# Kernel optimization log

Measured on AMD Instinct MI355X. Metric: run time of the kernel, lower is better.

The kernel has to match this reference:

```python
import jax, jax.numpy as jnp
import numpy as np

B, H, W = 2, 240, 320
C_ENC, C_SEG = 64, 21
TRUNC = 3
REP = 2 * TRUNC + 1
DMIN, DMAX = 0.4, 6.0
VOXEL = 0.03
FDIMS = 256.0
FX = FY = 300.0


def _point_sample(feat, grid):
    # feat: [C, Hf, Wf]; grid: [N, 2] = (x, y) in [0, 1].
    # Matches F.grid_sample(feat, 2*grid-1, bilinear, zeros, align_corners=False).
    Cc, Hf, Wf = feat.shape
    ix = grid[:, 0] * Wf - 0.5
    iy = grid[:, 1] * Hf - 0.5
    x0 = jnp.floor(ix)
    y0 = jnp.floor(iy)
    wx = ix - x0
    wy = iy - y0

    def gather(xi, yi):
        valid = (xi >= 0) & (xi < Wf) & (yi >= 0) & (yi < Hf)
        xc = jnp.clip(xi, 0, Wf - 1).astype(jnp.int32)
        yc = jnp.clip(yi, 0, Hf - 1).astype(jnp.int32)
        return feat[:, yc, xc] * valid.astype(feat.dtype)

    return (gather(x0, y0) * ((1 - wx) * (1 - wy))
            + gather(x0 + 1, y0) * (wx * (1 - wy))
            + gather(x0, y0 + 1) * ((1 - wx) * wy)
            + gather(x0 + 1, y0 + 1) * (wx * wy))  # [C, N]


def _single(depth, enc, seg, intr):
    f32 = depth.dtype
    K_inv = jnp.linalg.inv(intr)

    # generate_frustum: image corners unprojected at depth_min / depth_max.
    cpx = jnp.array([[0., 0.], [W, 0.], [0., H], [W, H]], f32)

    def unproj(z):
        p = jnp.concatenate([cpx * z, jnp.full((4, 1), z, f32), jnp.ones((4, 1), f32)], -1)
        return (K_inv @ p.T).T[:, :3]

    corners = jnp.concatenate([unproj(DMIN), unproj(DMAX)], 0)  # [8, 3]
    fmin = corners.min(0)
    fmax = corners.max(0)
    # compute_camera2frustum_transform: scale to voxels, shift frustum min to origin.
    c2f = (jnp.eye(4, dtype=f32)
           .at[jnp.arange(3), jnp.arange(3)].set(1.0 / VOXEL)
           .at[:3, 3].set(-fmin / VOXEL))
    pad_off = (FDIMS - (fmax - fmin) / VOXEL) * 0.5  # [3]

    # depth clipping (dense mask instead of nonzero; invalid rows zeroed at end)
    valid = (depth >= DMIN) & (depth <= DMAX)
    z = jnp.where(valid, depth, 0.0).reshape(-1)  # [N]
    yy, xx = jnp.meshgrid(jnp.arange(H, dtype=f32), jnp.arange(W, dtype=f32), indexing='ij')
    xy = jnp.stack([xx.reshape(-1), yy.reshape(-1)], -1)  # [N, 2] (x, y)
    norm_xy = xy / jnp.array([W, H], f32)
    xv_yv = norm_xy * jnp.array([W, H], f32) * z[:, None]  # image_size = (W, H)
    feat_grid = xy / jnp.array([W, H], f32)  # feat_size covers full image

    pix = jnp.concatenate([xv_yv, z[:, None], jnp.ones_like(z)[:, None]], -1).T  # [4, N]
    gc = (c2f @ (K_inv @ pix)).T[:, :3]  # [N, 3] frustum-grid coords
    cz = gc[:, 2]
    offs = jnp.arange(-TRUNC, TRUNC + 1, dtype=f32)  # [REP]
    coords = gc[:, None, :] + offs[None, :, None] * jnp.array([0., 0., 1.], f32)
    flat_coords = coords.reshape(-1, 3) + pad_off  # [N*REP, 3]

    # truncated df values: frac(z) + offset, then sign/abs channels
    df = (cz - jnp.trunc(cz))[:, None] + offs[None, :]  # [N, REP]
    df = jnp.stack([jnp.sign(df), jnp.abs(df)], -1)  # [N, REP, 2]

    seg_f = _point_sample(seg, norm_xy).T   # [N, C_SEG]
    enc_f = _point_sample(enc, feat_grid).T  # [N, C_ENC]
    samp = jnp.concatenate([enc_f, seg_f], -1)  # [N, C_ENC+C_SEG]
    samp = jnp.broadcast_to(samp[:, None, :], (H * W, REP, C_ENC + C_SEG))
    feats = jnp.concatenate([df, samp], -1).reshape(-1, 2 + C_ENC + C_SEG)  # [N*REP, D]

    m = jnp.broadcast_to(valid.reshape(-1)[:, None], (H * W, REP)).reshape(-1, 1).astype(f32)
    return jnp.concatenate([feats * m, flat_coords * m], -1)  # [N*REP, D+3]


def setup_inputs() -> dict:
    key = jax.random.key(0)
    k1, k2, k3 = jax.random.split(key, 3)
    depth = jax.random.uniform(k1, (B, H, W), minval=0.2, maxval=6.2)
    enc = jax.random.normal(k2, (B, C_ENC, H // 2, W // 2), dtype=jnp.float32)
    seg = jax.random.normal(k3, (B, C_SEG, H, W), dtype=jnp.float32)
    K = np.eye(4, dtype=np.float32)
    K[0, 0] = FX; K[1, 1] = FY; K[0, 2] = W / 2.0; K[1, 2] = H / 2.0
    intrinsic = jnp.asarray(np.broadcast_to(K, (B, 4, 4)).copy())
    return {"depth": depth, "encoder_features": enc, "sem_seg": seg, "intrinsic": intrinsic}


def reference(depth, encoder_features, sem_seg, intrinsic):
    # [B, H*W*REP, 2 + C_ENC + C_SEG + 3] = sparse features ++ frustum coordinates
    return jax.vmap(_single)(depth, encoder_features, sem_seg, intrinsic)
```

## Files before the change

### kernel.cpp

```cpp
#include <hip/hip_runtime.h>
#include <math.h>

#define BPIX 64
#define HW   76800
#define W_   320
#define H_   240
#define ENC_W 160
#define ENC_H 120
#define CENC 64
#define CSEG 21
#define NCH  85
#define ROW  90
#define PIXF 630
#define TPLS 94
#define NF4  10080

typedef float f4v __attribute__((ext_vector_type(4)));

__global__ void setup_consts_kernel(const float* __restrict__ intr,
                                    float* __restrict__ C) {
  int b = threadIdx.x;
  if (b >= 2) return;
  float A[4][4], inv[4][4];
  for (int r = 0; r < 4; ++r)
    for (int c = 0; c < 4; ++c) {
      A[r][c] = intr[b * 16 + r * 4 + c];
      inv[r][c] = (r == c) ? 1.f : 0.f;
    }
  for (int k = 0; k < 4; ++k) {
    int piv = k; float best = fabsf(A[k][k]);
    for (int r = k + 1; r < 4; ++r) {
      float v = fabsf(A[r][k]);
      if (v > best) { best = v; piv = r; }
    }
    if (piv != k) {
      for (int c = 0; c < 4; ++c) {
        float t = A[k][c]; A[k][c] = A[piv][c]; A[piv][c] = t;
        t = inv[k][c]; inv[k][c] = inv[piv][c]; inv[piv][c] = t;
      }
    }
    float ip = 1.f / A[k][k];
    for (int c = 0; c < 4; ++c) { A[k][c] *= ip; inv[k][c] *= ip; }
    for (int r = 0; r < 4; ++r) if (r != k) {
      float f = A[r][k];
      for (int c = 0; c < 4; ++c) { A[r][c] -= f * A[k][c]; inv[r][c] -= f * inv[k][c]; }
    }
  }
  const float cpx[4][2] = {{0.f, 0.f}, {320.f, 0.f}, {0.f, 240.f}, {320.f, 240.f}};
  float fmn[3] = {1e30f, 1e30f, 1e30f}, fmx[3] = {-1e30f, -1e30f, -1e30f};
  for (int zi = 0; zi < 2; ++zi) {
    float z = zi ? 6.0f : 0.4f;
    for (int i = 0; i < 4; ++i) {
      float px = cpx[i][0] * z, py = cpx[i][1] * z;
      for (int ax = 0; ax < 3; ++ax) {
        float v = inv[ax][0] * px + inv[ax][1] * py + inv[ax][2] * z + inv[ax][3];
        fmn[ax] = fminf(fmn[ax], v);
        fmx[ax] = fmaxf(fmx[ax], v);
      }
    }
  }
  float* Cb = C + b * 32;
  for (int r = 0; r < 4; ++r)
    for (int c = 0; c < 4; ++c) Cb[r * 4 + c] = inv[r][c];
  for (int ax = 0; ax < 3; ++ax) {
    Cb[16 + ax] = -fmn[ax] / 0.03f;
    Cb[19 + ax] = (256.0f - (fmx[ax] - fmn[ax]) / 0.03f) * 0.5f;
  }
}

__global__ __launch_bounds__(256) void sparse_proj_kernel(
    const float* __restrict__ depth, const float* __restrict__ enc,
    const float* __restrict__ seg, const float* __restrict__ C,
    float* __restrict__ out) {
  __shared__ float  tpl[BPIX * TPLS];
  __shared__ float2 sd[BPIX * 7];
  __shared__ float  fcz[BPIX * 7];
  __shared__ float  mArr[BPIX];
  __shared__ int    eo0[BPIX], eo1[BPIX], eo2[BPIX], eo3[BPIX];
  __shared__ float  ew0[BPIX], ew1[BPIX], ew2[BPIX], ew3[BPIX];
  __shared__ int    so0[BPIX], so1[BPIX], so2[BPIX], so3[BPIX];
  __shared__ float  sw0[BPIX], sw1[BPIX], sw2[BPIX], sw3[BPIX];

  const int tid = threadIdx.x;
  const int bx  = blockIdx.x;
  const int b   = blockIdx.y;
  const float* Cb = C + b * 32;
  const int x0 = (bx % 5) * 64;
  const int yrow = bx / 5;

  const int grp = tid >> 6;
  const int p   = tid & 63;

  if (grp == 0) {
    const float d = depth[(size_t)b * HW + bx * BPIX + p];
    const bool val = (d >= 0.4f) && (d <= 6.0f);
    const float m = val ? 1.f : 0.f;
    const float z = val ? d : 0.f;
    const float nx = (float)(x0 + p) / 320.f;
    const float ny = (float)yrow / 240.f;
    const float xv = nx * 320.f * z;
    const float yv = ny * 240.f * z;
    const float q0 = Cb[0] * xv + Cb[1] * yv + Cb[2] * z + Cb[3];
    const float q1 = Cb[4] * xv + Cb[5] * yv + Cb[6] * z + Cb[7];
    const float q2 = Cb[8] * xv + Cb[9] * yv + Cb[10] * z + Cb[11];
    const float q3 = Cb[12] * xv + Cb[13] * yv + Cb[14] * z + Cb[15];
    const float INV_V = (float)(1.0 / 0.03);
    const float gcx = q0 * INV_V + Cb[16] * q3;
    const float gcy = q1 * INV_V + Cb[17] * q3;
    const float gcz = q2 * INV_V + Cb[18] * q3;
    mArr[p] = m;
    tpl[p * TPLS + 87] = (gcx + Cb[19]) * m;
    tpl[p * TPLS + 88] = (gcy + Cb[20]) * m;
    const float fr = gcz - truncf(gcz);
    const float fz = (gcz + Cb[21]) * m;
#pragma unroll
    for (int r = 0; r < 7; ++r) {
      const float df = fr + (float)(r - 3);
      const float s = (df > 0.f) ? 1.f : ((df < 0.f) ? -1.f : 0.f);
      sd[p * 7 + r] = make_float2(s * m, fabsf(df) * m);
      fcz[p * 7 + r] = fz + (float)(r - 3) * m;
    }
  } else if (grp == 1) {
    const float nx = (float)(x0 + p) / 320.f;
    const float ny = (float)yrow / 240.f;
    const float ix = nx * 160.f - 0.5f;
    const float iy = ny * 120.f - 0.5f;
    const float x0f = floorf(ix), y0f = floorf(iy);
    const float wx = ix - x0f, wy = iy - y0f;
    const int xi0 = (int)x0f, yi0 = (int)y0f;
    const int xi1 = xi0 + 1, yi1 = yi0 + 1;
    const float vx0 = (xi0 >= 0 && xi0 < ENC_W) ? 1.f : 0.f;
    const float vx1 = (xi1 >= 0 && xi1 < ENC_W) ? 1.f : 0.f;
    const float vy0 = (yi0 >= 0 && yi0 < ENC_H) ? 1.f : 0.f;
    const float vy1 = (yi1 >= 0 && yi1 < ENC_H) ? 1.f : 0.f;
    const int xc0 = min(max(xi0, 0), ENC_W - 1), xc1 = min(max(xi1, 0), ENC_W - 1);
    const int yc0 = min(max(yi0, 0), ENC_H - 1), yc1 = min(max(yi1, 0), ENC_H - 1);
    eo0[p] = yc0 * ENC_W + xc0; ew0[p] = (1.f - wx) * (1.f - wy) * vx0 * vy0;
    eo1[p] = yc0 * ENC_W + xc1; ew1[p] = wx * (1.f - wy) * vx1 * vy0;
    eo2[p] = yc1 * ENC_W + xc0; ew2[p] = (1.f - wx) * wy * vx0 * vy1;
    eo3[p] = yc1 * ENC_W + xc1; ew3[p] = wx * wy * vx1 * vy1;
  } else if (grp == 2) {
    const float nx = (float)(x0 + p) / 320.f;
    const float ny = (float)yrow / 240.f;
    const float ix = nx * 320.f - 0.5f;
    const float iy = ny * 240.f - 0.5f;
    const float x0f = floorf(ix), y0f = floorf(iy);
    const float wx = ix - x0f, wy = iy - y0f;
    const int xi0 = (int)x0f, yi0 = (int)y0f;
    const int xi1 = xi0 + 1, yi1 = yi0 + 1;
    const float vx0 = (xi0 >= 0 && xi0 < W_) ? 1.f : 0.f;
    const float vx1 = (xi1 >= 0 && xi1 < W_) ? 1.f : 0.f;
    const float vy0 = (yi0 >= 0 && yi0 < H_) ? 1.f : 0.f;
    const float vy1 = (yi1 >= 0 && yi1 < H_) ? 1.f : 0.f;
    const int xc0 = min(max(xi0, 0), W_ - 1), xc1 = min(max(xi1, 0), W_ - 1);
    const int yc0 = min(max(yi0, 0), H_ - 1), yc1 = min(max(yi1, 0), H_ - 1);
    so0[p] = yc0 * W_ + xc0; sw0[p] = (1.f - wx) * (1.f - wy) * vx0 * vy0;
    so1[p] = yc0 * W_ + xc1; sw1[p] = wx * (1.f - wy) * vx1 * vy0;
    so2[p] = yc1 * W_ + xc0; sw2[p] = (1.f - wx) * wy * vx0 * vy1;
    so3[p] = yc1 * W_ + xc1; sw3[p] = wx * wy * vx1 * vy1;
  }
  __syncthreads();

  for (int idx = tid; idx < BPIX * NCH; idx += 256) {
    const int pp = idx & (BPIX - 1);
    const int ch = idx >> 6;
    float v;
    if (ch < CENC) {
      const float* fb = enc + ((size_t)b * CENC + ch) * (ENC_H * ENC_W);
      v = ew0[pp] * fb[eo0[pp]] + ew1[pp] * fb[eo1[pp]] +
          ew2[pp] * fb[eo2[pp]] + ew3[pp] * fb[eo3[pp]];
    } else {
      const float* fb = seg + ((size_t)b * CSEG + (ch - CENC)) * (size_t)HW;
      v = sw0[pp] * fb[so0[pp]] + sw1[pp] * fb[so1[pp]] +
          sw2[pp] * fb[so2[pp]] + sw3[pp] * fb[so3[pp]];
    }
    tpl[pp * TPLS + 2 + ch] = v * mArr[pp];
  }
  __syncthreads();

  f4v* out4 = reinterpret_cast<f4v*>(out + (size_t)(b * HW + bx * BPIX) * PIXF);
  for (int j = tid; j < NF4; j += 256) {
    const unsigned e0 = (unsigned)j << 2;
    const int pq = (int)((e0 * 53262u) >> 25);
    const int w  = (int)e0 - pq * 630;
    const int r  = (int)(((unsigned)w * 729u) >> 16);
    const int c  = w - r * 90;
    f4v v;
    if ((unsigned)(c - 2) <= 83u) {
      const float2* t = reinterpret_cast<const float2*>(&tpl[pq * TPLS + c]);
      const float2 a = t[0];
      const float2 bq = t[1];
      v.x = a.x; v.y = a.y; v.z = bq.x; v.w = bq.y;
    } else {
#pragma unroll
      for (int k = 0; k < 4; ++k) {
        const unsigned e = e0 + (unsigned)k;
        const int pk = (int)((e * 53262u) >> 25);
        const int wk = (int)e - pk * 630;
        const int rk = (int)(((unsigned)wk * 729u) >> 16);
        const int ck = wk - rk * 90;
        float val;
        if (ck == 0)       val = sd[pk * 7 + rk].x;
        else if (ck == 1)  val = sd[pk * 7 + rk].y;
        else if (ck == 89) val = fcz[pk * 7 + rk];
        else               val = tpl[pk * TPLS + ck];
        v[k] = val;
      }
    }
    __builtin_nontemporal_store(v, &out4[j]);
  }
}

extern "C" void kernel_launch(void* const* d_in, const int* in_sizes, int n_in,
                              void* d_out, int out_size, void* d_ws, size_t ws_size,
                              hipStream_t stream) {
  const float* depth = (const float*)d_in[0];
  const float* enc   = (const float*)d_in[1];
  const float* seg   = (const float*)d_in[2];
  const float* intr  = (const float*)d_in[3];
  float* out = (float*)d_out;
  float* C   = (float*)d_ws;

  setup_consts_kernel<<<1, 64, 0, stream>>>(intr, C);
  dim3 grid(HW / BPIX, 2);
  sparse_proj_kernel<<<grid, 256, 0, stream>>>(depth, enc, seg, C, out);
}
```

Before: 463.3 us.

## Write output as float2 per pixel-column with 7 replicas per thread

The store loop changes from coalesced float4 nontemporal stores, which decode pixel, replica and column per element, to one thread per (pixel, float2 column) that reads shared memory once and writes the value to all 7 replica rows. The per-replica sign, distance and z data are now computed inside the store loop instead of being staged in shared memory. This cuts shared-memory reads and index arithmetic. In exchange it uses narrower 8-byte stores strided across the 630-float row, drops the nontemporal hint, and weakens coalescing.

```diff
diff --git a/kernel.cpp b/kernel.cpp
--- a/kernel.cpp
+++ b/kernel.cpp
@@ -13,9 +13,7 @@
 #define ROW  90
 #define PIXF 630
 #define TPLS 94
-#define NF4  10080
-
-typedef float f4v __attribute__((ext_vector_type(4)));
+#define NT2  2880
 
 __global__ void setup_consts_kernel(const float* __restrict__ intr,
                                     float* __restrict__ C) {
@@ -72,20 +70,18 @@
     const float* __restrict__ depth, const float* __restrict__ enc,
     const float* __restrict__ seg, const float* __restrict__ C,
     float* __restrict__ out) {
-  __shared__ float  tpl[BPIX * TPLS];
-  __shared__ float2 sd[BPIX * 7];
-  __shared__ float  fcz[BPIX * 7];
-  __shared__ float  mArr[BPIX];
-  __shared__ int    eo0[BPIX], eo1[BPIX], eo2[BPIX], eo3[BPIX];
-  __shared__ float  ew0[BPIX], ew1[BPIX], ew2[BPIX], ew3[BPIX];
-  __shared__ int    so0[BPIX], so1[BPIX], so2[BPIX], so3[BPIX];
-  __shared__ float  sw0[BPIX], sw1[BPIX], sw2[BPIX], sw3[BPIX];
+  __shared__ float tpl[BPIX * TPLS];
+  __shared__ float mArr[BPIX], frArr[BPIX], fzArr[BPIX];
+  __shared__ int   eo0[BPIX], eo1[BPIX], eo2[BPIX], eo3[BPIX];
+  __shared__ float ew0[BPIX], ew1[BPIX], ew2[BPIX], ew3[BPIX];
+  __shared__ int   so0[BPIX], so1[BPIX], so2[BPIX], so3[BPIX];
+  __shared__ float sw0[BPIX], sw1[BPIX], sw2[BPIX], sw3[BPIX];
 
   const int tid = threadIdx.x;
   const int bx  = blockIdx.x;
   const int b   = blockIdx.y;
   const float* Cb = C + b * 32;
-  const int x0 = (bx % 5) * 64;
+  const int x0   = (bx % 5) * 64;
   const int yrow = bx / 5;
 
   const int grp = tid >> 6;
@@ -108,18 +104,11 @@
     const float gcx = q0 * INV_V + Cb[16] * q3;
     const float gcy = q1 * INV_V + Cb[17] * q3;
     const float gcz = q2 * INV_V + Cb[18] * q3;
-    mArr[p] = m;
+    mArr[p]  = m;
+    frArr[p] = gcz - truncf(gcz);
+    fzArr[p] = (gcz + Cb[21]) * m;
     tpl[p * TPLS + 87] = (gcx + Cb[19]) * m;
     tpl[p * TPLS + 88] = (gcy + Cb[20]) * m;
-    const float fr = gcz - truncf(gcz);
-    const float fz = (gcz + Cb[21]) * m;
-#pragma unroll
-    for (int r = 0; r < 7; ++r) {
-      const float df = fr + (float)(r - 3);
-      const float s = (df > 0.f) ? 1.f : ((df < 0.f) ? -1.f : 0.f);
-      sd[p * 7 + r] = make_float2(s * m, fabsf(df) * m);
-      fcz[p * 7 + r] = fz + (float)(r - 3) * m;
-    }
   } else if (grp == 1) {
     const float nx = (float)(x0 + p) / 320.f;
     const float ny = (float)yrow / 240.f;
@@ -178,36 +167,32 @@
   }
   __syncthreads();
 
-  f4v* out4 = reinterpret_cast<f4v*>(out + (size_t)(b * HW + bx * BPIX) * PIXF);
-  for (int j = tid; j < NF4; j += 256) {
-    const unsigned e0 = (unsigned)j << 2;
-    const int pq = (int)((e0 * 53262u) >> 25);
-    const int w  = (int)e0 - pq * 630;
-    const int r  = (int)(((unsigned)w * 729u) >> 16);
-    const int c  = w - r * 90;
-    f4v v;
-    if ((unsigned)(c - 2) <= 83u) {
-      const float2* t = reinterpret_cast<const float2*>(&tpl[pq * TPLS + c]);
-      const float2 a = t[0];
-      const float2 bq = t[1];
-      v.x = a.x; v.y = a.y; v.z = bq.x; v.w = bq.y;
+  float* const base_out = out + (size_t)(b * HW + bx * BPIX) * PIXF;
+  for (int t = tid; t < NT2; t += 256) {
+    const int pq = t / 45;
+    const int c2 = t - pq * 45;
+    float2* dst = reinterpret_cast<float2*>(base_out + pq * PIXF + c2 * 2);
+    if (c2 == 0) {
+      const float m = mArr[pq], fr = frArr[pq];
+#pragma unroll
+      for (int r = 0; r < 7; ++r) {
+        const float df = fr + (float)(r - 3);
+        const float s = (df > 0.f) ? 1.f : ((df < 0.f) ? -1.f : 0.f);
+        dst[r * 45] = make_float2(s * m, fabsf(df) * m);
+      }
+    } else if (c2 == 44) {
+      const float m = mArr[pq];
+      const float fy = tpl[pq * TPLS + 88];
+      const float fz = fzArr[pq];
+#pragma unroll
+      for (int r = 0; r < 7; ++r)
+        dst[r * 45] = make_float2(fy, fz + (float)(r - 3) * m);
     } else {
+      const float2 v = *reinterpret_cast<const float2*>(&tpl[pq * TPLS + 2 * c2]);
 #pragma unroll
-      for (int k = 0; k < 4; ++k) {
-        const unsigned e = e0 + (unsigned)k;
-        const int pk = (int)((e * 53262u) >> 25);
-        const int wk = (int)e - pk * 630;
-        const int rk = (int)(((unsigned)wk * 729u) >> 16);
-        const int ck = wk - rk * 90;
-        float val;
-        if (ck == 0)       val = sd[pk * 7 + rk].x;
-        else if (ck == 1)  val = sd[pk * 7 + rk].y;
-        else if (ck == 89) val = fcz[pk * 7 + rk];
-        else               val = tpl[pk * TPLS + ck];
-        v[k] = val;
-      }
-    }
-    __builtin_nontemporal_store(v, &out4[j]);
+      for (int r = 0; r < 7; ++r)
+        dst[r * 45] = v;
+    }
   }
 }
 
```

After: 473.1 us. 2.1% more time.
